# Kernel optimization log

Hardware: AMD Instinct MI355X
Metric: run time of the kernel (lower is better)

Reference implementation:

```python
import jax, jax.numpy as jnp
import numpy as np

FEATURE_DIM = 1024
N_CONCEPTS = 32768
BATCH = 1024
TEMPERATURE = 0.1
EPS = 1e-12  # matches torch F.normalize eps


def l2_normalize(x, axis=-1):
    n = jnp.linalg.norm(x, axis=axis, keepdims=True)
    return x / jnp.maximum(n, EPS)


def setup_inputs() -> dict:
    key = jax.random.key(0)
    k1, k2, k3, k4 = jax.random.split(key, 4)
    features = jax.random.normal(k1, (BATCH, FEATURE_DIM), dtype=jnp.float32)
    # Linear projection params (original inits to identity/zeros; random exercises the math)
    W = jnp.eye(FEATURE_DIM, dtype=jnp.float32) + 0.02 * jax.random.normal(k2, (FEATURE_DIM, FEATURE_DIM), dtype=jnp.float32)
    b = 0.01 * jax.random.normal(k3, (FEATURE_DIM,), dtype=jnp.float32)
    prototypes = l2_normalize(jax.random.normal(k4, (N_CONCEPTS, FEATURE_DIM), dtype=jnp.float32))
    return {"features": features, "W": W, "b": b, "prototypes": prototypes}


def reference(features, W, b, prototypes):
    # projection: features @ W.T + b   (torch nn.Linear convention)
    projected = jnp.einsum('bd,ed->be', features, W) + b          # [B, D]
    projected = l2_normalize(projected)                           # [B, D]
    # cosine similarity against all prototypes
    similarities = jnp.einsum('bd,kd->bk', projected, prototypes) # [B, K]
    activations = jax.nn.softmax(similarities / TEMPERATURE, axis=-1)
    best_idx = jnp.argmax(similarities, axis=-1)                  # [B] int
    return activations, best_idx
```

## Files before the change

### kernel.cpp

```cpp
#include <hip/hip_runtime.h>
#include <hip/hip_bf16.h>


typedef __attribute__((ext_vector_type(8))) short short8;
typedef __attribute__((ext_vector_type(4))) float floatx4;

__device__ __forceinline__ unsigned short f2bf(float f) {
  unsigned int u = __float_as_uint(f);
  u += 0x7fffu + ((u >> 16) & 1u);
  return (unsigned short)(u >> 16);
}
__device__ __forceinline__ float bf2f(unsigned short h) {
  return __uint_as_float(((unsigned int)h) << 16);
}

__global__ __launch_bounds__(256) void cvt_f32_bf16(
    const float* __restrict__ src, unsigned short* __restrict__ dst, int n8) {
  int i = blockIdx.x * blockDim.x + threadIdx.x;
  if (i >= n8) return;
  const float4* s4 = (const float4*)src;
  float4 a = s4[2 * i];
  float4 b = s4[2 * i + 1];
  short8 o;
  o[0] = (short)f2bf(a.x); o[1] = (short)f2bf(a.y);
  o[2] = (short)f2bf(a.z); o[3] = (short)f2bf(a.w);
  o[4] = (short)f2bf(b.x); o[5] = (short)f2bf(b.y);
  o[6] = (short)f2bf(b.z); o[7] = (short)f2bf(b.w);
  ((short8*)dst)[i] = o;
}

__global__ __launch_bounds__(256) void cvt_split3(
    const float* __restrict__ src, unsigned short* __restrict__ H,
    unsigned short* __restrict__ Md, unsigned short* __restrict__ L, int n4) {
  int i = blockIdx.x * blockDim.x + threadIdx.x;
  if (i >= n4) return;
  float4 x = ((const float4*)src)[i];
  ushort4 h, m, l;
  float v, r;
  v = x.x; h.x = f2bf(v); r = v - bf2f(h.x); m.x = f2bf(r); l.x = f2bf(r - bf2f(m.x));
  v = x.y; h.y = f2bf(v); r = v - bf2f(h.y); m.y = f2bf(r); l.y = f2bf(r - bf2f(m.y));
  v = x.z; h.z = f2bf(v); r = v - bf2f(h.z); m.z = f2bf(r); l.z = f2bf(r - bf2f(m.z));
  v = x.w; h.w = f2bf(v); r = v - bf2f(h.w); m.w = f2bf(r); l.w = f2bf(r - bf2f(m.w));
  ((ushort4*)H)[i] = h; ((ushort4*)Md)[i] = m; ((ushort4*)L)[i] = l;
}

__global__ __launch_bounds__(256) void gemm_nt_bf16(
    const unsigned short* __restrict__ A, const unsigned short* __restrict__ B,
    float* __restrict__ C, int M, int N, int K) {
  __shared__ unsigned short As[128 * 32];
  __shared__ unsigned short Bs[128 * 32];
  const int tid  = threadIdx.x;
  const int wave = tid >> 6;
  const int lane = tid & 63;
  const long tm = (long)blockIdx.y * 128;
  const long tn = (long)blockIdx.x * 128;
  const int wm = (wave & 1) * 64;
  const int wn = (wave >> 1) * 64;

  floatx4 acc[4][4];
#pragma unroll
  for (int i = 0; i < 4; i++)
#pragma unroll
    for (int j = 0; j < 4; j++) acc[i][j] = (floatx4){0.f, 0.f, 0.f, 0.f};

  const int rstage = tid >> 2;
  const int cstage = (tid & 3) * 8;
  const unsigned short* Abase = A + (tm + rstage) * (long)K + cstage;
  const unsigned short* Bbase = B + (tn + rstage) * (long)K + cstage;

  for (int k0 = 0; k0 < K; k0 += 32) {
    __builtin_amdgcn_global_load_lds(
        (const __attribute__((address_space(1))) void*)(Abase + k0),
        (__attribute__((address_space(3))) void*)(As + wave * 512), 16, 0, 0);
    __builtin_amdgcn_global_load_lds(
        (const __attribute__((address_space(1))) void*)(Abase + 64 * (long)K + k0),
        (__attribute__((address_space(3))) void*)(As + 2048 + wave * 512), 16, 0, 0);
    __builtin_amdgcn_global_load_lds(
        (const __attribute__((address_space(1))) void*)(Bbase + k0),
        (__attribute__((address_space(3))) void*)(Bs + wave * 512), 16, 0, 0);
    __builtin_amdgcn_global_load_lds(
        (const __attribute__((address_space(1))) void*)(Bbase + 64 * (long)K + k0),
        (__attribute__((address_space(3))) void*)(Bs + 2048 + wave * 512), 16, 0, 0);
    __syncthreads();

    short8 af[4], bfv[4];
    const int fr = lane & 15;
    const int koff = (lane >> 4) * 8;
#pragma unroll
    for (int mf = 0; mf < 4; mf++)
      af[mf] = *(const short8*)(As + (wm + mf * 16 + fr) * 32 + koff);
#pragma unroll
    for (int nf = 0; nf < 4; nf++)
      bfv[nf] = *(const short8*)(Bs + (wn + nf * 16 + fr) * 32 + koff);
#pragma unroll
    for (int mf = 0; mf < 4; mf++)
#pragma unroll
      for (int nf = 0; nf < 4; nf++)
        acc[mf][nf] = __builtin_amdgcn_mfma_f32_16x16x32_bf16(
            af[mf], bfv[nf], acc[mf][nf], 0, 0, 0);
    __syncthreads();
  }

  const long crow = tm + wm + ((lane >> 4) * 4);
  const long ccol = tn + wn + (lane & 15);
#pragma unroll
  for (int mf = 0; mf < 4; mf++)
#pragma unroll
    for (int nf = 0; nf < 4; nf++)
#pragma unroll
      for (int r = 0; r < 4; r++)
        C[(crow + mf * 16 + r) * (long)N + ccol + nf * 16] = acc[mf][nf][r];
}

__global__ __launch_bounds__(256) void gemm_split6_nt(
    const unsigned short* __restrict__ Ah, const unsigned short* __restrict__ Am,
    const unsigned short* __restrict__ Al, const unsigned short* __restrict__ Bh,
    const unsigned short* __restrict__ Bm, const unsigned short* __restrict__ Bl,
    float* __restrict__ C, int M, int N, int K) {
  __shared__ unsigned short sA[3][64 * 32];
  __shared__ unsigned short sB[3][64 * 32];
  const int tid  = threadIdx.x;
  const int wave = tid >> 6;
  const int lane = tid & 63;
  const long tm = (long)blockIdx.y * 64;
  const long tn = (long)blockIdx.x * 64;
  const int wm = (wave & 1) * 32;
  const int wn = (wave >> 1) * 32;

  floatx4 accH[2][2], accL[2][2];
#pragma unroll
  for (int i = 0; i < 2; i++)
#pragma unroll
    for (int j = 0; j < 2; j++) {
      accH[i][j] = (floatx4){0.f, 0.f, 0.f, 0.f};
      accL[i][j] = (floatx4){0.f, 0.f, 0.f, 0.f};
    }

  const int rstage = tid >> 2;
  const int cstage = (tid & 3) * 8;
  const long aoff = (tm + rstage) * (long)K + cstage;
  const long boff = (tn + rstage) * (long)K + cstage;
  const unsigned short* Asrc[3] = {Ah + aoff, Am + aoff, Al + aoff};
  const unsigned short* Bsrc[3] = {Bh + boff, Bm + boff, Bl + boff};

  for (int k0 = 0; k0 < K; k0 += 32) {
#pragma unroll
    for (int p = 0; p < 3; p++) {
      __builtin_amdgcn_global_load_lds(
          (const __attribute__((address_space(1))) void*)(Asrc[p] + k0),
          (__attribute__((address_space(3))) void*)(sA[p] + wave * 512), 16, 0, 0);
      __builtin_amdgcn_global_load_lds(
          (const __attribute__((address_space(1))) void*)(Bsrc[p] + k0),
          (__attribute__((address_space(3))) void*)(sB[p] + wave * 512), 16, 0, 0);
    }
    __syncthreads();

    const int fr = lane & 15;
    const int koff = (lane >> 4) * 8;
    short8 a_[3][2], b_[3][2];
#pragma unroll
    for (int p = 0; p < 3; p++)
#pragma unroll
      for (int mf = 0; mf < 2; mf++) {
        a_[p][mf] = *(const short8*)(sA[p] + (wm + mf * 16 + fr) * 32 + koff);
        b_[p][mf] = *(const short8*)(sB[p] + (wn + mf * 16 + fr) * 32 + koff);
      }
#pragma unroll
    for (int mf = 0; mf < 2; mf++)
#pragma unroll
      for (int nf = 0; nf < 2; nf++) {
        accH[mf][nf] = __builtin_amdgcn_mfma_f32_16x16x32_bf16(
            a_[0][mf], b_[0][nf], accH[mf][nf], 0, 0, 0);
        accL[mf][nf] = __builtin_amdgcn_mfma_f32_16x16x32_bf16(
            a_[0][mf], b_[1][nf], accL[mf][nf], 0, 0, 0);
        accL[mf][nf] = __builtin_amdgcn_mfma_f32_16x16x32_bf16(
            a_[1][mf], b_[0][nf], accL[mf][nf], 0, 0, 0);
        accL[mf][nf] = __builtin_amdgcn_mfma_f32_16x16x32_bf16(
            a_[0][mf], b_[2][nf], accL[mf][nf], 0, 0, 0);
        accL[mf][nf] = __builtin_amdgcn_mfma_f32_16x16x32_bf16(
            a_[2][mf], b_[0][nf], accL[mf][nf], 0, 0, 0);
        accL[mf][nf] = __builtin_amdgcn_mfma_f32_16x16x32_bf16(
            a_[1][mf], b_[1][nf], accL[mf][nf], 0, 0, 0);
      }
    __syncthreads();
  }

  const long crow = tm + wm + ((lane >> 4) * 4);
  const long ccol = tn + wn + (lane & 15);
#pragma unroll
  for (int mf = 0; mf < 2; mf++)
#pragma unroll
    for (int nf = 0; nf < 2; nf++)
#pragma unroll
      for (int r = 0; r < 4; r++)
        C[(crow + mf * 16 + r) * (long)N + ccol + nf * 16] =
            accH[mf][nf][r] + accL[mf][nf][r];
}

__global__ __launch_bounds__(256) void norm_bias_rows(
    const float* __restrict__ P, const float* __restrict__ bias,
    unsigned short* __restrict__ Pn, float* __restrict__ Pn32) {
  const int b = blockIdx.x, tid = threadIdx.x;
  float4 v = ((const float4*)(P + (long)b * 1024))[tid];
  float4 bb = ((const float4*)bias)[tid];
  v.x += bb.x; v.y += bb.y; v.z += bb.z; v.w += bb.w;
  float ss = v.x * v.x + v.y * v.y + v.z * v.z + v.w * v.w;
#pragma unroll
  for (int off = 32; off > 0; off >>= 1) ss += __shfl_down(ss, off);
  __shared__ float wred[4];
  if ((tid & 63) == 0) wred[tid >> 6] = ss;
  __syncthreads();
  float tot = wred[0] + wred[1] + wred[2] + wred[3];
  float inv = 1.0f / fmaxf(sqrtf(tot), 1e-12f);
  float4 p = make_float4(v.x * inv, v.y * inv, v.z * inv, v.w * inv);
  ((float4*)Pn32)[b * 256 + tid] = p;
  ushort4 o;
  o.x = f2bf(p.x); o.y = f2bf(p.y); o.z = f2bf(p.z); o.w = f2bf(p.w);
  ((ushort4*)Pn)[b * 256 + tid] = o;
}

__global__ __launch_bounds__(256) void softmax_argmax_refine(
    float* __restrict__ S, const float* __restrict__ Pn32,
    const float* __restrict__ protos, float* __restrict__ idx_out) {
  const int b = blockIdx.x, tid = threadIdx.x;
  const int wave = tid >> 6, lane = tid & 63;
  float* row = S + (long)b * 32768;

  float m = -3.4e38f, l = 0.f;
  for (int i = tid; i < 32768; i += 256) {
    float z = row[i] * 10.0f;
    if (z > m) { l = l * __expf(m - z) + 1.0f; m = z; }
    else l += __expf(z - m);
  }
#pragma unroll
  for (int off = 32; off > 0; off >>= 1) {
    float mo = __shfl_down(m, off);
    float lo = __shfl_down(l, off);
    float M = fmaxf(m, mo);
    l = l * __expf(m - M) + lo * __expf(mo - M);
    m = M;
  }
  __shared__ float sm_[4], sl_[4];
  __shared__ int cand[128];
  __shared__ int ncand;
  if (lane == 0) { sm_[wave] = m; sl_[wave] = l; }
  if (tid == 0) ncand = 0;
  __syncthreads();
  float M = fmaxf(fmaxf(sm_[0], sm_[1]), fmaxf(sm_[2], sm_[3]));
  float L = sl_[0] * __expf(sm_[0] - M) + sl_[1] * __expf(sm_[1] - M) +
            sl_[2] * __expf(sm_[2] - M) + sl_[3] * __expf(sm_[3] - M);
  float invL = 1.0f / L;
  float thr = M * 0.1f - 0.012f;

  for (int i = tid; i < 32768; i += 256) {
    float s = row[i];
    row[i] = __expf(s * 10.0f - M) * invL;
    if (s >= thr) {
      int p = atomicAdd(&ncand, 1);
      if (p < 128) cand[p] = i;
    }
  }
  __syncthreads();
  int n = ncand < 128 ? ncand : 128;

  float4 pv = ((const float4*)(Pn32 + (long)b * 1024))[tid];
  __shared__ double dred[4];
  double best = -1e300;
  int besti = 0x7fffffff;
  for (int c = 0; c < n; c++) {
    int k = cand[c];
    float4 kv = ((const float4*)(protos + (long)k * 1024))[tid];
    double d = (double)pv.x * kv.x + (double)pv.y * kv.y +
               (double)pv.z * kv.z + (double)pv.w * kv.w;
#pragma unroll
    for (int off = 32; off > 0; off >>= 1) d += __shfl_down(d, off);
    if (lane == 0) dred[wave] = d;
    __syncthreads();
    if (tid == 0) {
      double tot = dred[0] + dred[1] + dred[2] + dred[3];
      if (tot > best || (tot == best && k < besti)) { best = tot; besti = k; }
    }
    __syncthreads();
  }
  if (tid == 0) idx_out[b] = (float)besti;
}

extern "C" void kernel_launch(void* const* d_in, const int* in_sizes, int n_in,
                              void* d_out, int out_size, void* d_ws, size_t ws_size,
                              hipStream_t stream) {
  const float* features = (const float*)d_in[0];
  const float* W        = (const float*)d_in[1];
  const float* bias     = (const float*)d_in[2];
  const float* protos   = (const float*)d_in[3];

  const size_t MB = 1024 * 1024;
  char* ws = (char*)d_ws;
  unsigned short* protoB = (unsigned short*)ws;
  unsigned short* Fh = (unsigned short*)(ws + 64 * MB);
  unsigned short* Fm = (unsigned short*)(ws + 66 * MB);
  unsigned short* Fl = (unsigned short*)(ws + 68 * MB);
  unsigned short* Wh = (unsigned short*)(ws + 70 * MB);
  unsigned short* Wm = (unsigned short*)(ws + 72 * MB);
  unsigned short* Wl = (unsigned short*)(ws + 74 * MB);
  float*          P  = (float*)(ws + 76 * MB);
  unsigned short* Pn   = (unsigned short*)(ws + 64 * MB);
  float*          Pn32 = (float*)(ws + 66 * MB);

  float* S = (float*)d_out;
  float* idx_out = S + (size_t)1024 * 32768;

  cvt_f32_bf16<<<16384, 256, 0, stream>>>(protos, protoB, 32768 * 1024 / 8);
  cvt_split3<<<1024, 256, 0, stream>>>(features, Fh, Fm, Fl, 1024 * 1024 / 4);
  cvt_split3<<<1024, 256, 0, stream>>>(W, Wh, Wm, Wl, 1024 * 1024 / 4);
  gemm_split6_nt<<<dim3(16, 16), 256, 0, stream>>>(Fh, Fm, Fl, Wh, Wm, Wl, P,
                                                   1024, 1024, 1024);
  norm_bias_rows<<<1024, 256, 0, stream>>>(P, bias, Pn, Pn32);
  gemm_nt_bf16<<<dim3(256, 8), 256, 0, stream>>>(Pn, protoB, S, 1024, 32768, 1024);
  softmax_argmax_refine<<<1024, 256, 0, stream>>>(S, Pn32, protos, idx_out);
}
```

Measured before the change: 489.4 us.

## Split-K the projection GEMM and vectorize the softmax/argmax passes

The small projection GEMM gains a K-split along gridDim.z, writing two partial outputs that the normalization kernel sums, so its 256-block grid doubles to fill more compute units. The softmax/argmax kernel now reads and writes rows as float4, uses an xor-butterfly wave reduction, and trims the candidate buffer to 64. The split costs an extra 4 MB partial buffer and only turns on when the workspace is large enough. Halving the candidate capacity could drop the true argmax when many prototypes fall near the threshold.

```diff
diff --git a/kernel.cpp b/kernel.cpp
--- a/kernel.cpp
+++ b/kernel.cpp
@@ -116,7 +116,7 @@
     const unsigned short* __restrict__ Ah, const unsigned short* __restrict__ Am,
     const unsigned short* __restrict__ Al, const unsigned short* __restrict__ Bh,
     const unsigned short* __restrict__ Bm, const unsigned short* __restrict__ Bl,
-    float* __restrict__ C, int M, int N, int K) {
+    float* __restrict__ Cpart, int M, int N, int K) {
   __shared__ unsigned short sA[3][64 * 32];
   __shared__ unsigned short sB[3][64 * 32];
   const int tid  = threadIdx.x;
@@ -126,6 +126,9 @@
   const long tn = (long)blockIdx.x * 64;
   const int wm = (wave & 1) * 32;
   const int wn = (wave >> 1) * 32;
+  const int ksize = K / gridDim.z;
+  const int kbase = blockIdx.z * ksize;
+  float* C = Cpart + (size_t)blockIdx.z * M * N;
 
   floatx4 accH[2][2], accL[2][2];
 #pragma unroll
@@ -143,7 +146,7 @@
   const unsigned short* Asrc[3] = {Ah + aoff, Am + aoff, Al + aoff};
   const unsigned short* Bsrc[3] = {Bh + boff, Bm + boff, Bl + boff};
 
-  for (int k0 = 0; k0 < K; k0 += 32) {
+  for (int k0 = kbase; k0 < kbase + ksize; k0 += 32) {
 #pragma unroll
     for (int p = 0; p < 3; p++) {
       __builtin_amdgcn_global_load_lds(
@@ -198,10 +201,15 @@
 }
 
 __global__ __launch_bounds__(256) void norm_bias_rows(
-    const float* __restrict__ P, const float* __restrict__ bias,
-    unsigned short* __restrict__ Pn, float* __restrict__ Pn32) {
+    const float* __restrict__ P0, const float* __restrict__ P1, int nparts,
+    const float* __restrict__ bias, unsigned short* __restrict__ Pn,
+    float* __restrict__ Pn32) {
   const int b = blockIdx.x, tid = threadIdx.x;
-  float4 v = ((const float4*)(P + (long)b * 1024))[tid];
+  float4 v = ((const float4*)(P0 + (long)b * 1024))[tid];
+  if (nparts == 2) {
+    float4 v1 = ((const float4*)(P1 + (long)b * 1024))[tid];
+    v.x += v1.x; v.y += v1.y; v.z += v1.z; v.w += v1.w;
+  }
   float4 bb = ((const float4*)bias)[tid];
   v.x += bb.x; v.y += bb.y; v.z += bb.z; v.w += bb.w;
   float ss = v.x * v.x + v.y * v.y + v.z * v.z + v.w * v.w;
@@ -224,44 +232,58 @@
     const float* __restrict__ protos, float* __restrict__ idx_out) {
   const int b = blockIdx.x, tid = threadIdx.x;
   const int wave = tid >> 6, lane = tid & 63;
-  float* row = S + (long)b * 32768;
+  float4* row4 = (float4*)(S + (long)b * 32768);
 
   float m = -3.4e38f, l = 0.f;
-  for (int i = tid; i < 32768; i += 256) {
-    float z = row[i] * 10.0f;
-    if (z > m) { l = l * __expf(m - z) + 1.0f; m = z; }
-    else l += __expf(z - m);
-  }
-#pragma unroll
-  for (int off = 32; off > 0; off >>= 1) {
-    float mo = __shfl_down(m, off);
-    float lo = __shfl_down(l, off);
-    float M = fmaxf(m, mo);
-    l = l * __expf(m - M) + lo * __expf(mo - M);
-    m = M;
+#pragma unroll 4
+  for (int it = 0; it < 32; it++) {
+    float4 v = row4[tid + 256 * it];
+    float zx = v.x * 10.f, zy = v.y * 10.f, zz = v.z * 10.f, zw = v.w * 10.f;
+    float m4 = fmaxf(fmaxf(zx, zy), fmaxf(zz, zw));
+    float nm = fmaxf(m, m4);
+    l = l * __expf(m - nm) + __expf(zx - nm) + __expf(zy - nm) +
+        __expf(zz - nm) + __expf(zw - nm);
+    m = nm;
+  }
+#pragma unroll
+  for (int off = 1; off < 64; off <<= 1) {
+    float mo = __shfl_xor(m, off);
+    float lo = __shfl_xor(l, off);
+    float nm = fmaxf(m, mo);
+    l = l * __expf(m - nm) + lo * __expf(mo - nm);
+    m = nm;
   }
   __shared__ float sm_[4], sl_[4];
-  __shared__ int cand[128];
+  __shared__ int cand[64];
   __shared__ int ncand;
   if (lane == 0) { sm_[wave] = m; sl_[wave] = l; }
   if (tid == 0) ncand = 0;
   __syncthreads();
-  float M = fmaxf(fmaxf(sm_[0], sm_[1]), fmaxf(sm_[2], sm_[3]));
-  float L = sl_[0] * __expf(sm_[0] - M) + sl_[1] * __expf(sm_[1] - M) +
-            sl_[2] * __expf(sm_[2] - M) + sl_[3] * __expf(sm_[3] - M);
+  float Mz = fmaxf(fmaxf(sm_[0], sm_[1]), fmaxf(sm_[2], sm_[3]));
+  float L = sl_[0] * __expf(sm_[0] - Mz) + sl_[1] * __expf(sm_[1] - Mz) +
+            sl_[2] * __expf(sm_[2] - Mz) + sl_[3] * __expf(sm_[3] - Mz);
   float invL = 1.0f / L;
-  float thr = M * 0.1f - 0.012f;
-
-  for (int i = tid; i < 32768; i += 256) {
-    float s = row[i];
-    row[i] = __expf(s * 10.0f - M) * invL;
-    if (s >= thr) {
-      int p = atomicAdd(&ncand, 1);
-      if (p < 128) cand[p] = i;
+  float thr = Mz * 0.1f - 0.012f;
+
+#pragma unroll 4
+  for (int it = 0; it < 32; it++) {
+    int i4 = tid + 256 * it;
+    float4 v = row4[i4];
+    if (fmaxf(fmaxf(v.x, v.y), fmaxf(v.z, v.w)) >= thr) {
+      if (v.x >= thr) { int p = atomicAdd(&ncand, 1); if (p < 64) cand[p] = i4 * 4; }
+      if (v.y >= thr) { int p = atomicAdd(&ncand, 1); if (p < 64) cand[p] = i4 * 4 + 1; }
+      if (v.z >= thr) { int p = atomicAdd(&ncand, 1); if (p < 64) cand[p] = i4 * 4 + 2; }
+      if (v.w >= thr) { int p = atomicAdd(&ncand, 1); if (p < 64) cand[p] = i4 * 4 + 3; }
     }
+    float4 e;
+    e.x = __expf(v.x * 10.f - Mz) * invL;
+    e.y = __expf(v.y * 10.f - Mz) * invL;
+    e.z = __expf(v.z * 10.f - Mz) * invL;
+    e.w = __expf(v.w * 10.f - Mz) * invL;
+    row4[i4] = e;
   }
   __syncthreads();
-  int n = ncand < 128 ? ncand : 128;
+  int n = ncand < 64 ? ncand : 64;
 
   float4 pv = ((const float4*)(Pn32 + (long)b * 1024))[tid];
   __shared__ double dred[4];
@@ -302,9 +324,12 @@
   unsigned short* Wh = (unsigned short*)(ws + 70 * MB);
   unsigned short* Wm = (unsigned short*)(ws + 72 * MB);
   unsigned short* Wl = (unsigned short*)(ws + 74 * MB);
-  float*          P  = (float*)(ws + 76 * MB);
+  float*          P0 = (float*)(ws + 76 * MB);
+  float*          P1 = (float*)(ws + 80 * MB);
   unsigned short* Pn   = (unsigned short*)(ws + 64 * MB);
   float*          Pn32 = (float*)(ws + 66 * MB);
+
+  const int ksplit = (ws_size >= 84 * MB) ? 2 : 1;
 
   float* S = (float*)d_out;
   float* idx_out = S + (size_t)1024 * 32768;
@@ -312,9 +337,9 @@
   cvt_f32_bf16<<<16384, 256, 0, stream>>>(protos, protoB, 32768 * 1024 / 8);
   cvt_split3<<<1024, 256, 0, stream>>>(features, Fh, Fm, Fl, 1024 * 1024 / 4);
   cvt_split3<<<1024, 256, 0, stream>>>(W, Wh, Wm, Wl, 1024 * 1024 / 4);
-  gemm_split6_nt<<<dim3(16, 16), 256, 0, stream>>>(Fh, Fm, Fl, Wh, Wm, Wl, P,
-                                                   1024, 1024, 1024);
-  norm_bias_rows<<<1024, 256, 0, stream>>>(P, bias, Pn, Pn32);
+  gemm_split6_nt<<<dim3(16, 16, ksplit), 256, 0, stream>>>(
+      Fh, Fm, Fl, Wh, Wm, Wl, P0, 1024, 1024, 1024);
+  norm_bias_rows<<<1024, 256, 0, stream>>>(P0, P1, ksplit, bias, Pn, Pn32);
   gemm_nt_bf16<<<dim3(256, 8), 256, 0, stream>>>(Pn, protoB, S, 1024, 32768, 1024);
   softmax_argmax_refine<<<1024, 256, 0, stream>>>(S, Pn32, protos, idx_out);
 }
```

Result: faster. 442.4 us (-9.6%).
